# Kernel optimization log

Measured on AMD Instinct MI355X. Metric: run time of the kernel, lower is better.

Reference implementation:

```python
import jax, jax.numpy as jnp
import numpy as np

NUM_EMBEDDINGS = 1024
EMBEDDING_DIM = 64


def setup_inputs() -> dict:
    key = jax.random.key(0)
    kx, kw = jax.random.split(key)
    x = jax.random.normal(kx, (16, 4096, EMBEDDING_DIM), dtype=jnp.float32)
    # torch init: uniform(-1/K, 1/K)
    bound = 1.0 / NUM_EMBEDDINGS
    weight = jax.random.uniform(kw, (NUM_EMBEDDINGS, EMBEDDING_DIM),
                                dtype=jnp.float32, minval=-bound, maxval=bound)
    return {"x": x, "weight": weight}


def reference(x, weight):
    flat_x = x.reshape(-1, EMBEDDING_DIM)                      # [N, D]
    x_sq = jnp.sum(flat_x ** 2, axis=1, keepdims=True)
    w_sq = jnp.sum(weight ** 2, axis=1)[None, :]
    distances = x_sq - 2.0 * (flat_x @ weight.T) + w_sq
    encoding_indices = jnp.argmin(distances, axis=1)           # [N]
    quantized = weight[encoding_indices]                       # [N, D]
    e_latent_loss = jnp.mean((jax.lax.stop_gradient(quantized) - flat_x) ** 2)
    q_latent_loss = jnp.mean((quantized - jax.lax.stop_gradient(flat_x)) ** 2)
    loss = q_latent_loss + 0.25 * e_latent_loss
    # straight-through estimator
    quantized = flat_x + jax.lax.stop_gradient(quantized - flat_x)
    return quantized.reshape(x.shape), encoding_indices, loss
```

## Files before the change

### kernel.cpp

```cpp
#include <hip/hip_runtime.h>
#include <math.h>

#define EMB_D 64
#define MARGIN 6.0e-5f
#define SBIAS 0.5f

typedef float  f32x4  __attribute__((ext_vector_type(4)));
typedef short  bf16x8 __attribute__((ext_vector_type(8)));

__device__ __forceinline__ unsigned short f2bf(float f) {
    unsigned int u = __float_as_uint(f);
    return (unsigned short)((u + 0x7FFFu + ((u >> 16) & 1u)) >> 16);
}
__device__ __forceinline__ float bf2f(unsigned short h) {
    return __uint_as_float(((unsigned int)h) << 16);
}

union Pack8 { ushort u[8]; bf16x8 v; uint4 q; };

__device__ __forceinline__ bf16x8 ldbf8(const unsigned short* p) {
    union { uint4 u; bf16x8 v; } c;
    c.u = *(const uint4*)p;
    return c.v;
}

__global__ __launch_bounds__(256)
void vq_prepw_kernel(const float* __restrict__ w,
                     unsigned short* __restrict__ wt_hi,
                     unsigned short* __restrict__ wt_lo,
                     float* __restrict__ wsq, float* __restrict__ loss_out,
                     int K) {
    const int i = blockIdx.x * 256 + threadIdx.x;
    if (i == 0) loss_out[0] = 0.f;
    if (i >= K * 8) return;
    const int krow = i >> 3, q = i & 7;
    const int dest = ((krow >> 6) << 9) + (((krow >> 4) & 3) << 7) + (q << 4)
                   + (krow & 15);
    const float* src = w + (size_t)krow * EMB_D + q * 8;
    Pack8 h, l;
#pragma unroll
    for (int j = 0; j < 8; ++j) {
        const float f = src[j];
        h.u[j] = f2bf(f);
        l.u[j] = f2bf(f - bf2f(h.u[j]));
    }
    ((uint4*)wt_hi)[dest] = h.q;
    ((uint4*)wt_lo)[dest] = l.q;

    if (i < K) {
        const float* wr = w + (size_t)i * EMB_D;
        float r[8];
#pragma unroll
        for (int j = 0; j < 8; ++j) r[j] = __fmul_rn(wr[j], wr[j]);
#pragma unroll
        for (int t = 1; t < 8; ++t)
#pragma unroll
            for (int j = 0; j < 8; ++j)
                r[j] = __fadd_rn(r[j], __fmul_rn(wr[t * 8 + j], wr[t * 8 + j]));
        float a = __fadd_rn(__fadd_rn(r[0], r[1]), __fadd_rn(r[2], r[3]));
        float b = __fadd_rn(__fadd_rn(r[4], r[5]), __fadd_rn(r[6], r[7]));
        wsq[i] = __fadd_rn(a, b);
    }
}

__global__ __launch_bounds__(256, 2)
void vq_fused_kernel(const float* __restrict__ x,
                     const unsigned short* __restrict__ wt_hi,
                     const unsigned short* __restrict__ wt_lo,
                     const float* __restrict__ wsq,
                     const float* __restrict__ w,
                     float* __restrict__ out, float* __restrict__ loss_out,
                     int K, int N, float scale) {
    const int tid  = threadIdx.x;
    const int lane = tid & 63;
    const int wave = tid >> 6;
    const int quad = lane >> 4;
    const int c16  = lane & 15;
    const int rowbase = blockIdx.x * 128 + wave * 32;

    __shared__ uint4 sh4[512];
    __shared__ uint4 sl4[512];
    __shared__ float wsq_lds[1024];
    __shared__ float M1[4][32][17], M2[4][32][17];
    __shared__ int   N1[4][32][17], N2[4][32][17];
    __shared__ int   kf[128], strow[128], k2row[128];

    Pack8 AH0[2], AL0[2], AH1[2], AL1[2];
#pragma unroll
    for (int t = 0; t < 2; ++t) {
        const float* xrow =
            x + (size_t)(rowbase + t * 16 + c16) * EMB_D + quad * 8;
#pragma unroll
        for (int j = 0; j < 8; ++j) {
            const float f0 = xrow[j];
            AH0[t].u[j] = f2bf(f0);
            AL0[t].u[j] = f2bf(f0 - bf2f(AH0[t].u[j]));
            const float f1 = xrow[32 + j];
            AH1[t].u[j] = f2bf(f1);
            AL1[t].u[j] = f2bf(f1 - bf2f(AH1[t].u[j]));
        }
    }

    {
        float4 wv = ((const float4*)wsq)[tid];
        wv.x += SBIAS; wv.y += SBIAS; wv.z += SBIAS; wv.w += SBIAS;
        ((float4*)wsq_lds)[tid] = wv;
    }

    unsigned s1v[2][4], s2v[2][4];
#pragma unroll
    for (int t = 0; t < 2; ++t)
#pragma unroll
        for (int i = 0; i < 4; ++i) { s1v[t][i] = 0xFFFFFFFFu; s2v[t][i] = 0xFFFFFFFFu; }

    const uint4* gh = (const uint4*)wt_hi;
    const uint4* gl = (const uint4*)wt_lo;
    uint4 ph0 = gh[tid], ph1 = gh[256 + tid];
    uint4 pl0 = gl[tid], pl1 = gl[256 + tid];

    const int nseg = K >> 6;
    for (int seg = 0; seg < nseg; ++seg) {
        sh4[tid] = ph0; sh4[256 + tid] = ph1;
        sl4[tid] = pl0; sl4[256 + tid] = pl1;
        __syncthreads();
        if (seg + 1 < nseg) {
            const int b = (seg + 1) * 512;
            ph0 = gh[b + tid]; ph1 = gh[b + 256 + tid];
            pl0 = gl[b + tid]; pl1 = gl[b + 256 + tid];
        }

#pragma unroll
        for (int s = 0; s < 4; ++s) {
            const unsigned short* shp = (const unsigned short*)sh4;
            const unsigned short* slp = (const unsigned short*)sl4;
            const bf16x8 bhi0 = ldbf8(shp + (s * 128 + lane) * 8);
            const bf16x8 bhi1 = ldbf8(shp + (s * 128 + 64 + lane) * 8);
            const bf16x8 blo0 = ldbf8(slp + (s * 128 + lane) * 8);
            const bf16x8 blo1 = ldbf8(slp + (s * 128 + 64 + lane) * 8);
            const float wqb = wsq_lds[seg * 64 + s * 16 + c16];
            const unsigned idx6 = (unsigned)(seg * 4 + s);

#pragma unroll
            for (int t = 0; t < 2; ++t) {
                f32x4 acc = {0.f, 0.f, 0.f, 0.f};
                acc = __builtin_amdgcn_mfma_f32_16x16x32_bf16(AL0[t].v, bhi0, acc, 0, 0, 0);
                acc = __builtin_amdgcn_mfma_f32_16x16x32_bf16(AH0[t].v, blo0, acc, 0, 0, 0);
                acc = __builtin_amdgcn_mfma_f32_16x16x32_bf16(AL1[t].v, bhi1, acc, 0, 0, 0);
                acc = __builtin_amdgcn_mfma_f32_16x16x32_bf16(AH1[t].v, blo1, acc, 0, 0, 0);
                acc = __builtin_amdgcn_mfma_f32_16x16x32_bf16(AH0[t].v, bhi0, acc, 0, 0, 0);
                acc = __builtin_amdgcn_mfma_f32_16x16x32_bf16(AH1[t].v, bhi1, acc, 0, 0, 0);
#pragma unroll
                for (int i = 0; i < 4; ++i) {
                    const float sc = fmaf(-2.0f, acc[i], wqb);
                    const unsigned p =
                        (__float_as_uint(sc) & 0xFFFFFFC0u) | idx6;
                    const unsigned m = p > s1v[t][i] ? p : s1v[t][i];
                    s2v[t][i] = s2v[t][i] < m ? s2v[t][i] : m;
                    s1v[t][i] = s1v[t][i] < p ? s1v[t][i] : p;
                }
            }
        }
        __syncthreads();
    }

#pragma unroll
    for (int t = 0; t < 2; ++t)
#pragma unroll
        for (int i = 0; i < 4; ++i) {
            const int r32 = t * 16 + quad * 4 + i;
            M1[wave][r32][c16] = __uint_as_float(s1v[t][i] & 0xFFFFFFC0u);
            N1[wave][r32][c16] = (int)(((s1v[t][i] & 63u) << 4) | (unsigned)c16);
            M2[wave][r32][c16] = __uint_as_float(s2v[t][i] & 0xFFFFFFC0u);
            N2[wave][r32][c16] = (int)(((s2v[t][i] & 63u) << 4) | (unsigned)c16);
        }
    __syncthreads();
    if (lane < 16) {
#pragma unroll
        for (int rep = 0; rep < 2; ++rep) {
            const int r = rep * 16 + lane;
            float g1 = INFINITY, g2 = INFINITY, g3 = INFINITY;
            int   gk1 = 0, gk2 = 0;
#pragma unroll
            for (int c = 0; c < 16; ++c) {
#pragma unroll
                for (int h = 0; h < 2; ++h) {
                    const float s = h == 0 ? M1[wave][r][c] : M2[wave][r][c];
                    const int   k = h == 0 ? N1[wave][r][c] : N2[wave][r][c];
                    if (s < g1)      { g3 = g2; g2 = g1; gk2 = gk1; g1 = s; gk1 = k; }
                    else if (s < g2) { g3 = g2; g2 = s; gk2 = k; }
                    else if (s < g3) { g3 = s; }
                }
            }
            const int lr = wave * 32 + r;
            kf[lr] = gk1;
            int st = 0;
            if (g2 - g1 <= MARGIN) st = (g3 - g1 > MARGIN) ? 1 : 2;
            strow[lr] = st;
            k2row[lr] = gk2;
        }
    }
    __syncthreads();

    if (tid < 128 && strow[tid] == 1) {
        const int row = blockIdx.x * 128 + tid;
        const int ka = kf[tid], kb = k2row[tid];
        const float4* xp = (const float4*)(x + (size_t)row * EMB_D);
        const float4* wa = (const float4*)(w + (size_t)ka * EMB_D);
        const float4* wb = (const float4*)(w + (size_t)kb * EMB_D);
        float r[8];
        double aa0 = 0, aa1 = 0, aa2 = 0, aa3 = 0;
        double ab0 = 0, ab1 = 0, ab2 = 0, ab3 = 0;
#pragma unroll
        for (int q = 0; q < 16; ++q) {
            const float4 xv = xp[q], va = wa[q], vb = wb[q];
            const int j = (q & 1) * 4;
            if (q < 2) {
                r[j + 0] = __fmul_rn(xv.x, xv.x);
                r[j + 1] = __fmul_rn(xv.y, xv.y);
                r[j + 2] = __fmul_rn(xv.z, xv.z);
                r[j + 3] = __fmul_rn(xv.w, xv.w);
            } else {
                r[j + 0] = __fadd_rn(r[j + 0], __fmul_rn(xv.x, xv.x));
                r[j + 1] = __fadd_rn(r[j + 1], __fmul_rn(xv.y, xv.y));
                r[j + 2] = __fadd_rn(r[j + 2], __fmul_rn(xv.z, xv.z));
                r[j + 3] = __fadd_rn(r[j + 3], __fmul_rn(xv.w, xv.w));
            }
            aa0 = fma((double)xv.x, (double)va.x, aa0);
            aa1 = fma((double)xv.y, (double)va.y, aa1);
            aa2 = fma((double)xv.z, (double)va.z, aa2);
            aa3 = fma((double)xv.w, (double)va.w, aa3);
            ab0 = fma((double)xv.x, (double)vb.x, ab0);
            ab1 = fma((double)xv.y, (double)vb.y, ab1);
            ab2 = fma((double)xv.z, (double)vb.z, ab2);
            ab3 = fma((double)xv.w, (double)vb.w, ab3);
        }
        const float xsq = __fadd_rn(
            __fadd_rn(__fadd_rn(r[0], r[1]), __fadd_rn(r[2], r[3])),
            __fadd_rn(__fadd_rn(r[4], r[5]), __fadd_rn(r[6], r[7])));
        const float mfa = (float)((aa0 + aa1) + (aa2 + aa3));
        const float mfb = (float)((ab0 + ab1) + (ab2 + ab3));
        const float sa = __fadd_rn(__fsub_rn(xsq, __fmul_rn(2.0f, mfa)), wsq[ka]);
        const float sb = __fadd_rn(__fsub_rn(xsq, __fmul_rn(2.0f, mfb)), wsq[kb]);
        int win = ka;
        if (sb < sa || (sb == sa && kb < ka)) win = kb;
        kf[tid] = win;
    }
    __syncthreads();

    __shared__ float4 xs4[16];
    __shared__ float  xsqs;
    __shared__ float  ls[256];
    __shared__ int    lk[256];
    for (int i = 0; i < 128; ++i) {
        if (strow[i] != 2) continue;
        const int row = blockIdx.x * 128 + i;
        if (tid < 16) xs4[tid] = ((const float4*)(x + (size_t)row * EMB_D))[tid];
        __syncthreads();
        if (tid == 0) {
            const float* xf = (const float*)xs4;
            float r[8];
#pragma unroll
            for (int j = 0; j < 8; ++j) r[j] = __fmul_rn(xf[j], xf[j]);
#pragma unroll
            for (int t = 1; t < 8; ++t)
#pragma unroll
                for (int j = 0; j < 8; ++j)
                    r[j] = __fadd_rn(r[j], __fmul_rn(xf[t * 8 + j], xf[t * 8 + j]));
            xsqs = __fadd_rn(
                __fadd_rn(__fadd_rn(r[0], r[1]), __fadd_rn(r[2], r[3])),
                __fadd_rn(__fadd_rn(r[4], r[5]), __fadd_rn(r[6], r[7])));
        }
        __syncthreads();
        const float xsq = xsqs;

        float bs = INFINITY;
        int   bk = K;
        for (int t = 0; t < 4; ++t) {
            const int k = wave * (K >> 2) + t * 64 + lane;
            const float4* wr4 = (const float4*)(w + (size_t)k * EMB_D);
            double a0 = 0.0, a1 = 0.0, a2 = 0.0, a3 = 0.0;
#pragma unroll
            for (int q = 0; q < EMB_D / 4; ++q) {
                const float4 xv = xs4[q];
                const float4 wv = wr4[q];
                a0 = fma((double)xv.x, (double)wv.x, a0);
                a1 = fma((double)xv.y, (double)wv.y, a1);
                a2 = fma((double)xv.z, (double)wv.z, a2);
                a3 = fma((double)xv.w, (double)wv.w, a3);
            }
            const float mf = (float)((a0 + a1) + (a2 + a3));
            const float t2 = __fsub_rn(xsq, __fmul_rn(2.0f, mf));
            const float sc = __fadd_rn(t2, wsq[k]);
            if (sc < bs || (sc == bs && k < bk)) { bs = sc; bk = k; }
        }
        ls[tid] = bs; lk[tid] = bk;
        __syncthreads();
        if (wave == 0) {
            float gs = ls[lane];
            int   gk = lk[lane];
#pragma unroll
            for (int c = 1; c < 4; ++c) {
                const float os = ls[c * 64 + lane];
                const int   ok = lk[c * 64 + lane];
                if (os < gs || (os == gs && ok < gk)) { gs = os; gk = ok; }
            }
#pragma unroll
            for (int off = 32; off > 0; off >>= 1) {
                const float os = __shfl_down(gs, off);
                const int   ok = __shfl_down(gk, off);
                if (os < gs || (os == gs && ok < gk)) { gs = os; gk = ok; }
            }
            if (lane == 0) kf[i] = gk;
        }
        __syncthreads();
    }

    if (tid < 128) {
        const int row = blockIdx.x * 128 + tid;
        out[(size_t)N * EMB_D + row] = (float)kf[tid];
    }
    float lpart = 0.f;
#pragma unroll
    for (int rep = 0; rep < 8; ++rep) {
        int f4   = rep * 256 + tid;
        int rr   = f4 >> 4;
        int c    = f4 & 15;
        int k    = kf[rr];
        int grow = blockIdx.x * 128 + rr;
        float4 wv = ((const float4*)(w + (size_t)k * EMB_D))[c];
        float4 xq = ((const float4*)(x + (size_t)grow * EMB_D))[c];
        ((float4*)out)[(size_t)grow * (EMB_D / 4) + c] = wv;
        float dx = wv.x - xq.x, dy = wv.y - xq.y;
        float dz = wv.z - xq.z, dw = wv.w - xq.w;
        lpart += dx * dx + dy * dy + dz * dz + dw * dw;
    }
#pragma unroll
    for (int off = 32; off > 0; off >>= 1) lpart += __shfl_down(lpart, off);
    __shared__ float lred[4];
    if (lane == 0) lred[wave] = lpart;
    __syncthreads();
    if (tid == 0)
        atomicAdd(loss_out, ((lred[0] + lred[1]) + (lred[2] + lred[3])) * scale);
}

extern "C" void kernel_launch(void* const* d_in, const int* in_sizes, int n_in,
                              void* d_out, int out_size, void* d_ws, size_t ws_size,
                              hipStream_t stream) {
    const float* x = (const float*)d_in[0];
    const float* w = (const float*)d_in[1];
    float* out = (float*)d_out;
    const int xsz = in_sizes[0];
    const int wsz = in_sizes[1];
    const int N   = xsz / EMB_D;
    const int K   = wsz / EMB_D;
    const int NB  = N / 128;
    float* loss_out = out + (size_t)N * EMB_D + N;

    float* wsq = (float*)d_ws;
    unsigned short* wt_hi = (unsigned short*)(wsq + K);
    unsigned short* wt_lo = wt_hi + (size_t)K * EMB_D;

    vq_prepw_kernel<<<(K * 8 + 255) / 256, 256, 0, stream>>>(w, wt_hi, wt_lo,
                                                             wsq, loss_out, K);
    vq_fused_kernel<<<NB, 256, 0, stream>>>(x, wt_hi, wt_lo, wsq, w, out,
                                            loss_out, K, N,
                                            1.25f / (float)xsz);
}
```

Baseline: 135.3 us.

## Halve block size to 64 rows, split MFMA chains, pack top-2 merge

Each block now covers 64 rows with 128 threads (two waves) instead of 128 rows with 256 threads, which doubles the grid to 1024 blocks so CUs are filled more evenly. Each thread stages twice as much codebook data per segment. The six-MFMA dependent chain is split into two independent accumulators that are summed at the end, to hide MFMA latency. The cross-lane top-3 merge now keeps packed unsigned keys in fewer LDS arrays, and one thread per row does the merge instead of 16 lanes looping twice. The cost is that each block reloads the whole codebook, so total codebook traffic from L2 doubles. The fallback exact-search loop also runs with fewer threads per row.

Result: slower. 169.9 us (+25.5%).

```diff
diff --git a/kernel.cpp b/kernel.cpp
--- a/kernel.cpp
+++ b/kernel.cpp
@@ -63,7 +63,7 @@
     }
 }
 
-__global__ __launch_bounds__(256, 2)
+__global__ __launch_bounds__(128, 2)
 void vq_fused_kernel(const float* __restrict__ x,
                      const unsigned short* __restrict__ wt_hi,
                      const unsigned short* __restrict__ wt_lo,
@@ -76,14 +76,14 @@
     const int wave = tid >> 6;
     const int quad = lane >> 4;
     const int c16  = lane & 15;
-    const int rowbase = blockIdx.x * 128 + wave * 32;
+    const int rowbase = blockIdx.x * 64 + wave * 32;
 
     __shared__ uint4 sh4[512];
     __shared__ uint4 sl4[512];
     __shared__ float wsq_lds[1024];
-    __shared__ float M1[4][32][17], M2[4][32][17];
-    __shared__ int   N1[4][32][17], N2[4][32][17];
-    __shared__ int   kf[128], strow[128], k2row[128];
+    __shared__ unsigned Mp1[2][32][19];
+    __shared__ unsigned Mp2[2][32][19];
+    __shared__ int kf[64], strow[64], k2row[64];
 
     Pack8 AH0[2], AL0[2], AH1[2], AL1[2];
 #pragma unroll
@@ -102,9 +102,12 @@
     }
 
     {
-        float4 wv = ((const float4*)wsq)[tid];
-        wv.x += SBIAS; wv.y += SBIAS; wv.z += SBIAS; wv.w += SBIAS;
-        ((float4*)wsq_lds)[tid] = wv;
+        float4 a = ((const float4*)wsq)[tid];
+        float4 b = ((const float4*)wsq)[128 + tid];
+        a.x += SBIAS; a.y += SBIAS; a.z += SBIAS; a.w += SBIAS;
+        b.x += SBIAS; b.y += SBIAS; b.z += SBIAS; b.w += SBIAS;
+        ((float4*)wsq_lds)[tid]       = a;
+        ((float4*)wsq_lds)[128 + tid] = b;
     }
 
     unsigned s1v[2][4], s2v[2][4];
@@ -115,18 +118,25 @@
 
     const uint4* gh = (const uint4*)wt_hi;
     const uint4* gl = (const uint4*)wt_lo;
-    uint4 ph0 = gh[tid], ph1 = gh[256 + tid];
-    uint4 pl0 = gl[tid], pl1 = gl[256 + tid];
+    uint4 ph[4], pl[4];
+#pragma unroll
+    for (int j = 0; j < 4; ++j) { ph[j] = gh[j * 128 + tid]; pl[j] = gl[j * 128 + tid]; }
 
     const int nseg = K >> 6;
     for (int seg = 0; seg < nseg; ++seg) {
-        sh4[tid] = ph0; sh4[256 + tid] = ph1;
-        sl4[tid] = pl0; sl4[256 + tid] = pl1;
+#pragma unroll
+        for (int j = 0; j < 4; ++j) {
+            sh4[j * 128 + tid] = ph[j];
+            sl4[j * 128 + tid] = pl[j];
+        }
         __syncthreads();
         if (seg + 1 < nseg) {
             const int b = (seg + 1) * 512;
-            ph0 = gh[b + tid]; ph1 = gh[b + 256 + tid];
-            pl0 = gl[b + tid]; pl1 = gl[b + 256 + tid];
+#pragma unroll
+            for (int j = 0; j < 4; ++j) {
+                ph[j] = gh[b + j * 128 + tid];
+                pl[j] = gl[b + j * 128 + tid];
+            }
         }
 
 #pragma unroll
@@ -142,21 +152,22 @@
 
 #pragma unroll
             for (int t = 0; t < 2; ++t) {
-                f32x4 acc = {0.f, 0.f, 0.f, 0.f};
-                acc = __builtin_amdgcn_mfma_f32_16x16x32_bf16(AL0[t].v, bhi0, acc, 0, 0, 0);
-                acc = __builtin_amdgcn_mfma_f32_16x16x32_bf16(AH0[t].v, blo0, acc, 0, 0, 0);
-                acc = __builtin_amdgcn_mfma_f32_16x16x32_bf16(AL1[t].v, bhi1, acc, 0, 0, 0);
-                acc = __builtin_amdgcn_mfma_f32_16x16x32_bf16(AH1[t].v, blo1, acc, 0, 0, 0);
-                acc = __builtin_amdgcn_mfma_f32_16x16x32_bf16(AH0[t].v, bhi0, acc, 0, 0, 0);
-                acc = __builtin_amdgcn_mfma_f32_16x16x32_bf16(AH1[t].v, bhi1, acc, 0, 0, 0);
+                f32x4 a0 = {0.f, 0.f, 0.f, 0.f};
+                f32x4 a1 = {0.f, 0.f, 0.f, 0.f};
+                a0 = __builtin_amdgcn_mfma_f32_16x16x32_bf16(AL0[t].v, bhi0, a0, 0, 0, 0);
+                a1 = __builtin_amdgcn_mfma_f32_16x16x32_bf16(AL1[t].v, bhi1, a1, 0, 0, 0);
+                a0 = __builtin_amdgcn_mfma_f32_16x16x32_bf16(AH0[t].v, blo0, a0, 0, 0, 0);
+                a1 = __builtin_amdgcn_mfma_f32_16x16x32_bf16(AH1[t].v, blo1, a1, 0, 0, 0);
+                a0 = __builtin_amdgcn_mfma_f32_16x16x32_bf16(AH0[t].v, bhi0, a0, 0, 0, 0);
+                a1 = __builtin_amdgcn_mfma_f32_16x16x32_bf16(AH1[t].v, bhi1, a1, 0, 0, 0);
 #pragma unroll
                 for (int i = 0; i < 4; ++i) {
-                    const float sc = fmaf(-2.0f, acc[i], wqb);
+                    const float sc = fmaf(-2.0f, a0[i] + a1[i], wqb);
                     const unsigned p =
                         (__float_as_uint(sc) & 0xFFFFFFC0u) | idx6;
-                    const unsigned m = p > s1v[t][i] ? p : s1v[t][i];
-                    s2v[t][i] = s2v[t][i] < m ? s2v[t][i] : m;
-                    s1v[t][i] = s1v[t][i] < p ? s1v[t][i] : p;
+                    const unsigned mx = p > s1v[t][i] ? p : s1v[t][i];
+                    s2v[t][i] = s2v[t][i] < mx ? s2v[t][i] : mx;
+                    s1v[t][i] = s1v[t][i] < p  ? s1v[t][i] : p;
                 }
             }
         }
@@ -168,41 +179,46 @@
 #pragma unroll
         for (int i = 0; i < 4; ++i) {
             const int r32 = t * 16 + quad * 4 + i;
-            M1[wave][r32][c16] = __uint_as_float(s1v[t][i] & 0xFFFFFFC0u);
-            N1[wave][r32][c16] = (int)(((s1v[t][i] & 63u) << 4) | (unsigned)c16);
-            M2[wave][r32][c16] = __uint_as_float(s2v[t][i] & 0xFFFFFFC0u);
-            N2[wave][r32][c16] = (int)(((s2v[t][i] & 63u) << 4) | (unsigned)c16);
+            Mp1[wave][r32][c16] = s1v[t][i];
+            Mp2[wave][r32][c16] = s2v[t][i];
         }
     __syncthreads();
-    if (lane < 16) {
-#pragma unroll
-        for (int rep = 0; rep < 2; ++rep) {
-            const int r = rep * 16 + lane;
-            float g1 = INFINITY, g2 = INFINITY, g3 = INFINITY;
-            int   gk1 = 0, gk2 = 0;
-#pragma unroll
-            for (int c = 0; c < 16; ++c) {
-#pragma unroll
-                for (int h = 0; h < 2; ++h) {
-                    const float s = h == 0 ? M1[wave][r][c] : M2[wave][r][c];
-                    const int   k = h == 0 ? N1[wave][r][c] : N2[wave][r][c];
-                    if (s < g1)      { g3 = g2; g2 = g1; gk2 = gk1; g1 = s; gk1 = k; }
-                    else if (s < g2) { g3 = g2; g2 = s; gk2 = k; }
-                    else if (s < g3) { g3 = s; }
-                }
-            }
-            const int lr = wave * 32 + r;
-            kf[lr] = gk1;
-            int st = 0;
-            if (g2 - g1 <= MARGIN) st = (g3 - g1 > MARGIN) ? 1 : 2;
-            strow[lr] = st;
-            k2row[lr] = gk2;
-        }
+    if (tid < 64) {
+        const int wv = tid >> 5, r = tid & 31;
+        unsigned g1 = 0xFFFFFFFFu, g2 = 0xFFFFFFFFu, g3 = 0xFFFFFFFFu;
+        int gk1 = 0, gk2 = 0;
+#pragma unroll
+        for (int c = 0; c < 16; ++c) {
+            {
+                const unsigned p = Mp1[wv][r][c];
+                if (p < g1)      { g3 = g2; g2 = g1; gk2 = gk1; g1 = p;
+                                   gk1 = (int)(((p & 63u) << 4) | (unsigned)c); }
+                else if (p < g2) { g3 = g2; g2 = p;
+                                   gk2 = (int)(((p & 63u) << 4) | (unsigned)c); }
+                else if (p < g3) { g3 = p; }
+            }
+            {
+                const unsigned p = Mp2[wv][r][c];
+                if (p < g1)      { g3 = g2; g2 = g1; gk2 = gk1; g1 = p;
+                                   gk1 = (int)(((p & 63u) << 4) | (unsigned)c); }
+                else if (p < g2) { g3 = g2; g2 = p;
+                                   gk2 = (int)(((p & 63u) << 4) | (unsigned)c); }
+                else if (p < g3) { g3 = p; }
+            }
+        }
+        kf[tid] = gk1;
+        const float f1 = __uint_as_float(g1 & 0xFFFFFFC0u);
+        const float f2 = __uint_as_float(g2 & 0xFFFFFFC0u);
+        const float f3 = __uint_as_float(g3 & 0xFFFFFFC0u);
+        int st = 0;
+        if (f2 - f1 <= MARGIN) st = (f3 - f1 > MARGIN) ? 1 : 2;
+        strow[tid] = st;
+        k2row[tid] = gk2;
     }
     __syncthreads();
 
-    if (tid < 128 && strow[tid] == 1) {
-        const int row = blockIdx.x * 128 + tid;
+    if (tid < 64 && strow[tid] == 1) {
+        const int row = blockIdx.x * 64 + tid;
         const int ka = kf[tid], kb = k2row[tid];
         const float4* xp = (const float4*)(x + (size_t)row * EMB_D);
         const float4* wa = (const float4*)(w + (size_t)ka * EMB_D);
@@ -249,11 +265,11 @@
 
     __shared__ float4 xs4[16];
     __shared__ float  xsqs;
-    __shared__ float  ls[256];
-    __shared__ int    lk[256];
-    for (int i = 0; i < 128; ++i) {
+    __shared__ float  ls[128];
+    __shared__ int    lk[128];
+    for (int i = 0; i < 64; ++i) {
         if (strow[i] != 2) continue;
-        const int row = blockIdx.x * 128 + i;
+        const int row = blockIdx.x * 64 + i;
         if (tid < 16) xs4[tid] = ((const float4*)(x + (size_t)row * EMB_D))[tid];
         __syncthreads();
         if (tid == 0) {
@@ -275,8 +291,8 @@
 
         float bs = INFINITY;
         int   bk = K;
-        for (int t = 0; t < 4; ++t) {
-            const int k = wave * (K >> 2) + t * 64 + lane;
+        for (int t = 0; t < 8; ++t) {
+            const int k = t * 128 + tid;
             const float4* wr4 = (const float4*)(w + (size_t)k * EMB_D);
             double a0 = 0.0, a1 = 0.0, a2 = 0.0, a3 = 0.0;
 #pragma unroll
@@ -298,10 +314,9 @@
         if (wave == 0) {
             float gs = ls[lane];
             int   gk = lk[lane];
-#pragma unroll
-            for (int c = 1; c < 4; ++c) {
-                const float os = ls[c * 64 + lane];
-                const int   ok = lk[c * 64 + lane];
+            {
+                const float os = ls[64 + lane];
+                const int   ok = lk[64 + lane];
                 if (os < gs || (os == gs && ok < gk)) { gs = os; gk = ok; }
             }
 #pragma unroll
@@ -315,18 +330,18 @@
         __syncthreads();
     }
 
-    if (tid < 128) {
-        const int row = blockIdx.x * 128 + tid;
+    if (tid < 64) {
+        const int row = blockIdx.x * 64 + tid;
         out[(size_t)N * EMB_D + row] = (float)kf[tid];
     }
     float lpart = 0.f;
 #pragma unroll
     for (int rep = 0; rep < 8; ++rep) {
-        int f4   = rep * 256 + tid;
+        int f4   = rep * 128 + tid;
         int rr   = f4 >> 4;
         int c    = f4 & 15;
         int k    = kf[rr];
-        int grow = blockIdx.x * 128 + rr;
+        int grow = blockIdx.x * 64 + rr;
         float4 wv = ((const float4*)(w + (size_t)k * EMB_D))[c];
         float4 xq = ((const float4*)(x + (size_t)grow * EMB_D))[c];
         ((float4*)out)[(size_t)grow * (EMB_D / 4) + c] = wv;
@@ -336,11 +351,11 @@
     }
 #pragma unroll
     for (int off = 32; off > 0; off >>= 1) lpart += __shfl_down(lpart, off);
-    __shared__ float lred[4];
+    __shared__ float lred[2];
     if (lane == 0) lred[wave] = lpart;
     __syncthreads();
     if (tid == 0)
-        atomicAdd(loss_out, ((lred[0] + lred[1]) + (lred[2] + lred[3])) * scale);
+        atomicAdd(loss_out, (lred[0] + lred[1]) * scale);
 }
 
 extern "C" void kernel_launch(void* const* d_in, const int* in_sizes, int n_in,
@@ -353,7 +368,7 @@
     const int wsz = in_sizes[1];
     const int N   = xsz / EMB_D;
     const int K   = wsz / EMB_D;
-    const int NB  = N / 128;
+    const int NB  = N / 64;
     float* loss_out = out + (size_t)N * EMB_D + N;
 
     float* wsq = (float*)d_ws;
@@ -362,7 +377,7 @@
 
     vq_prepw_kernel<<<(K * 8 + 255) / 256, 256, 0, stream>>>(w, wt_hi, wt_lo,
                                                              wsq, loss_out, K);
-    vq_fused_kernel<<<NB, 256, 0, stream>>>(x, wt_hi, wt_lo, wsq, w, out,
+    vq_fused_kernel<<<NB, 128, 0, stream>>>(x, wt_hi, wt_lo, wsq, w, out,
                                             loss_out, K, N,
                                             1.25f / (float)xsz);
 }
```
